# Kernel optimization log

Hardware: AMD Instinct MI355X
Metric: run time of the kernel (lower is better)

## Reference

```python
import jax, jax.numpy as jnp
import numpy as np
import math

B, N, F = 16, 1024, 1024
OUT = 1024

def setup_inputs() -> dict:
    key = jax.random.key(0)
    k1, k2, k3, k4 = jax.random.split(key, 4)
    prott5_emd = jax.random.normal(k1, (B, N, F), dtype=jnp.float32)
    # shared (dense) normalized adjacency, as the original applies one adj to every sample
    adj = jax.random.uniform(k2, (N, N), dtype=jnp.float32)
    adj = adj / jnp.sum(adj, axis=1, keepdims=True)  # row-normalize like a GCN propagation matrix
    h0 = jax.random.normal(k3, (B, N, F), dtype=jnp.float32)
    stdv = 1.0 / math.sqrt(OUT)
    weight = jax.random.uniform(k4, (F, OUT), minval=-stdv, maxval=stdv, dtype=jnp.float32)
    return {"prott5_emd": prott5_emd, "adj": adj, "h0": h0, "weight": weight,
            "lamda": 0.5, "alpha": 0.1, "l": 1}

def reference(prott5_emd, adj, h0, weight, lamda, alpha, l):
    # GraphConvolution (GCNII-style), variant=False, residual=False
    theta = min(1.0, math.log(lamda / l + 1.0))  # static python scalar
    # batched aggregation: adj @ x_i for every sample i  ->  [B, N, F]
    hi = jnp.einsum('nm,bmf->bnf', adj, prott5_emd)
    support = (1.0 - alpha) * hi + alpha * h0          # affine combine with initial features
    out = theta * jnp.einsum('bnf,fo->bno', support, weight) + (1.0 - theta) * support
    return out
```

## Files before the change

### kernel.cpp

```cpp
#include <hip/hip_runtime.h>
#include <hip/hip_bf16.h>

typedef __attribute__((ext_vector_type(8))) short bf16x8;
typedef __attribute__((ext_vector_type(4))) float f32x4;
typedef __attribute__((ext_vector_type(4))) unsigned int u32x4;
typedef __attribute__((ext_vector_type(2))) unsigned int u32x2;

__device__ __forceinline__ float b2f(unsigned short u) {
  unsigned int x = ((unsigned int)u) << 16;
  float f;
  __builtin_memcpy(&f, &x, 4);
  return f;
}
__device__ __forceinline__ unsigned short f2b(float f) {
  __hip_bfloat16 h = __float2bfloat16(f);
  unsigned short u;
  __builtin_memcpy(&u, &h, 2);
  return u;
}

__global__ __launch_bounds__(256) void prep_all(
    const float* __restrict__ X, const float* __restrict__ adj,
    const float* __restrict__ W, unsigned short* __restrict__ XT,
    unsigned short* __restrict__ AJ, unsigned short* __restrict__ WT,
    float theta) {
  const int z = blockIdx.z;
  const int t = threadIdx.x;
  const int r0 = blockIdx.y * 64, c0 = blockIdx.x * 64;

  if (z == 17) {
#pragma unroll
    for (int p = 0; p < 4; ++p) {
      const int id = t + 256 * p;
      const int r = id >> 4, c4 = (id & 15) * 4;
      f32x4 v = *(const f32x4*)(adj + (size_t)(r0 + r) * 1024 + (c0 + c4));
      unsigned short o[4];
#pragma unroll
      for (int j = 0; j < 4; ++j) o[j] = f2b(v[j]);
      u32x2 pk;
      __builtin_memcpy(&pk, o, 8);
      *(u32x2*)(AJ + (size_t)(r0 + r) * 1024 + (c0 + c4)) = pk;
    }
    return;
  }

  if (z == 16) {
    __shared__ float tile[64][65];
#pragma unroll
    for (int p = 0; p < 4; ++p) {
      const int id = t + 256 * p;
      const int r = id >> 4, c4 = (id & 15) * 4;
      f32x4 v = *(const f32x4*)(W + (size_t)(r0 + r) * 1024 + (c0 + c4));
#pragma unroll
      for (int j = 0; j < 4; ++j) tile[r][c4 + j] = v[j];
    }
    __syncthreads();
#pragma unroll
    for (int p = 0; p < 2; ++p) {
      const int id = t + 256 * p;
      const int oc = id >> 3, cr8 = (id & 7) * 8;
      u32x4 v;
      unsigned short* pv = (unsigned short*)&v;
#pragma unroll
      for (int j = 0; j < 8; ++j) {
        const int o = c0 + oc, f = r0 + cr8 + j;
        float val = theta * tile[cr8 + j][oc] + (o == f ? (1.0f - theta) : 0.f);
        pv[j] = f2b(val);
      }
      *(u32x4*)(WT + (size_t)(c0 + oc) * 1024 + (r0 + cr8)) = v;
    }
    return;
  }

  __shared__ unsigned short tile[64][68];
  const float* s = X + (size_t)z * 1024 * 1024;
  unsigned short* d = XT + (size_t)z * 1024 * 1024;
#pragma unroll
  for (int p = 0; p < 4; ++p) {
    const int id = t + 256 * p;
    const int r = id >> 4, c4 = (id & 15) * 4;
    f32x4 v = *(const f32x4*)(s + (size_t)(r0 + r) * 1024 + (c0 + c4));
#pragma unroll
    for (int j = 0; j < 4; ++j) tile[r][c4 + j] = f2b(v[j]);
  }
  __syncthreads();
#pragma unroll
  for (int p = 0; p < 2; ++p) {
    const int id = t + 256 * p;
    const int oc = id >> 3, cr8 = (id & 7) * 8;
    u32x4 v;
    unsigned short* pv = (unsigned short*)&v;
#pragma unroll
    for (int j = 0; j < 8; ++j) pv[j] = tile[cr8 + j][oc];
    *(u32x4*)(d + (size_t)(c0 + oc) * 1024 + (r0 + cr8)) = v;
  }
}

__global__ __launch_bounds__(256, 3) void gemm1(
    const unsigned short* __restrict__ A, const unsigned short* __restrict__ BT,
    const float* __restrict__ E, unsigned short* __restrict__ Cq,
    float c0, float c1) {
  constexpr int NT = 16;
  constexpr size_t NF = 1024ull * 1024ull;
  __shared__ unsigned short Abuf[128 * 64];
  __shared__ unsigned short Bbuf[128 * 64];
  const int bid = blockIdx.x;
  const int nid = (bid & 7) * 128 + (bid >> 3);
  const size_t m0 = (size_t)(nid >> 7) * 128, n0 = (size_t)(nid & 127) * 128;
  const int t = threadIdx.x, lane = t & 63, wv = t >> 6;
  const int wm = (wv >> 1) * 64, wn = (wv & 1) * 64;

  f32x4 acc[4][4];
#pragma unroll
  for (int i = 0; i < 4; ++i)
#pragma unroll
    for (int j = 0; j < 4; ++j) acc[i][j] = (f32x4){0.f, 0.f, 0.f, 0.f};

  for (int tt = 0; tt < NT; ++tt) {
    const int k0 = tt * 64;
#pragma unroll
    for (int l = 0; l < 4; ++l) {
      const int id = l * 256 + t;
      const int rl = id >> 3, c = id & 7;
      const int gc = (c ^ (rl & 7)) << 3;
      const unsigned short* ga = A + (m0 + rl) * 1024 + k0 + gc;
      __builtin_amdgcn_global_load_lds(
          (const __attribute__((address_space(1))) unsigned int*)ga,
          (__attribute__((address_space(3))) unsigned int*)(Abuf + id * 8),
          16, 0, 0);
    }
#pragma unroll
    for (int l = 0; l < 4; ++l) {
      const int id = l * 256 + t;
      const int rl = id >> 3, c = id & 7;
      const int gc = (c ^ (rl & 7)) << 3;
      const unsigned short* gb = BT + (n0 + rl) * 1024 + k0 + gc;
      __builtin_amdgcn_global_load_lds(
          (const __attribute__((address_space(1))) unsigned int*)gb,
          (__attribute__((address_space(3))) unsigned int*)(Bbuf + id * 8),
          16, 0, 0);
    }
    asm volatile("s_waitcnt vmcnt(0)" ::: "memory");
    __builtin_amdgcn_s_barrier();

    bf16x8 breg[4][2];
#pragma unroll
    for (int nj = 0; nj < 4; ++nj)
#pragma unroll
      for (int kk = 0; kk < 2; ++kk) {
        const int row = wn + nj * 16 + (lane & 15);
        const int ch = ((kk * 4 + (lane >> 4)) ^ (row & 7)) << 3;
        breg[nj][kk] = *(const bf16x8*)(Bbuf + row * 64 + ch);
      }
#pragma unroll
    for (int mi = 0; mi < 4; ++mi) {
      bf16x8 ar[2];
#pragma unroll
      for (int kk = 0; kk < 2; ++kk) {
        const int row = wm + mi * 16 + (lane & 15);
        const int ch = ((kk * 4 + (lane >> 4)) ^ (row & 7)) << 3;
        ar[kk] = *(const bf16x8*)(Abuf + row * 64 + ch);
      }
#pragma unroll
      for (int nj = 0; nj < 4; ++nj)
#pragma unroll
        for (int kk = 0; kk < 2; ++kk)
          acc[mi][nj] = __builtin_amdgcn_mfma_f32_16x16x32_bf16(
              ar[kk], breg[nj][kk], acc[mi][nj], 0, 0, 0);
    }
    __builtin_amdgcn_s_barrier();
  }

  const size_t base = (n0 >> 10) * NF + (n0 & 1023) + m0 * 1024;
  float* ldsF = (float*)Abuf;
#pragma unroll
  for (int NH = 0; NH < 2; ++NH) {
    __syncthreads();
    if ((wv & 1) == NH) {
      const int q = lane >> 4;
#pragma unroll
      for (int mi = 0; mi < 4; ++mi)
#pragma unroll
        for (int nj = 0; nj < 4; ++nj)
#pragma unroll
          for (int r = 0; r < 4; ++r) {
            const int row = wm + mi * 16 + q * 4 + r;
            const int col = (nj * 16 + (lane & 15)) ^ (q << 4);
            ldsF[row * 64 + col] = acc[mi][nj][r];
          }
    }
    __syncthreads();
#pragma unroll 4
    for (int it = 0; it < 8; ++it) {
      const int chunk = it * 256 + t;
      const int row = chunk >> 4;
      const int c4 = (chunk & 15) * 4;
      const int sc4 = c4 ^ (((row >> 2) & 3) << 4);
      const f32x4 s = *(const f32x4*)(ldsF + row * 64 + sc4);
      const size_t goff = base + (size_t)row * 1024 + NH * 64 + c4;
      const f32x4 h = *(const f32x4*)(E + goff);
      unsigned short o[4];
#pragma unroll
      for (int j = 0; j < 4; ++j) o[j] = f2b(c0 * s[j] + c1 * h[j]);
      u32x2 pk;
      __builtin_memcpy(&pk, o, 8);
      *(u32x2*)(Cq + goff) = pk;
    }
  }
}

__device__ __forceinline__ void stage_tile16(unsigned short* ldsbase,
                                             const unsigned short* __restrict__ gbase,
                                             size_t rowbase, int half, int k0,
                                             int t, int wv) {
#pragma unroll
  for (int l = 0; l < 2; ++l) {
    const int id = l * 512 + t;
    const int rl = id >> 3, c = id & 7;
    const int gc = (c ^ (rl & 7)) << 3;
    const unsigned short* g = gbase + (rowbase + half * 128 + rl) * 1024 + k0 + gc;
    unsigned short* dst = ldsbase + half * 8192 + (l * 512 + wv * 64) * 8;
    __builtin_amdgcn_global_load_lds(
        (const __attribute__((address_space(1))) unsigned int*)g,
        (__attribute__((address_space(3))) unsigned int*)dst, 16, 0, 0);
  }
}

#define LOAD_A(MH)                                                     \
  {                                                                    \
    const unsigned short* Ard = lds[rd * 2 + 0];                       \
    _Pragma("unroll") for (int mi = 0; mi < 4; ++mi)                   \
        _Pragma("unroll") for (int kk = 0; kk < 2; ++kk) {             \
      const int row = wm + (MH)*64 + mi * 16 + (lane & 15);            \
      const int ch = ((kk * 4 + (lane >> 4)) ^ (row & 7)) << 3;        \
      areg[mi][kk] = *(const bf16x8*)(Ard + row * 64 + ch);            \
    }                                                                  \
  }
#define LOAD_B(NH, BR)                                                 \
  {                                                                    \
    const unsigned short* Brd = lds[rd * 2 + 1];                       \
    _Pragma("unroll") for (int nj = 0; nj < 2; ++nj)                   \
        _Pragma("unroll") for (int kk = 0; kk < 2; ++kk) {             \
      const int row = wn + (NH)*32 + nj * 16 + (lane & 15);            \
      const int ch = ((kk * 4 + (lane >> 4)) ^ (row & 7)) << 3;        \
      BR[nj][kk] = *(const bf16x8*)(Brd + row * 64 + ch);              \
    }                                                                  \
  }
#define MFMA_Q(MH, NH, BR)                                             \
  do {                                                                 \
    __builtin_amdgcn_s_setprio(1);                                     \
    _Pragma("unroll") for (int mi = 0; mi < 4; ++mi)                   \
        _Pragma("unroll") for (int nj = 0; nj < 2; ++nj)               \
            _Pragma("unroll") for (int kk = 0; kk < 2; ++kk)           \
        acc[(MH)*4 + mi][(NH)*2 + nj] =                                \
        __builtin_amdgcn_mfma_f32_16x16x32_bf16(                       \
            areg[mi][kk], BR[nj][kk], acc[(MH)*4 + mi][(NH)*2 + nj],   \
            0, 0, 0);                                                  \
    __builtin_amdgcn_s_setprio(0);                                     \
  } while (0)
#define LGKM0                                          \
  asm volatile("s_waitcnt lgkmcnt(0)" ::: "memory");   \
  __builtin_amdgcn_sched_barrier(0)
#define BAR __builtin_amdgcn_s_barrier()

__global__ __launch_bounds__(512, 2) void gemm2(
    const unsigned short* __restrict__ A, const unsigned short* __restrict__ BT,
    float* __restrict__ Co) {
  constexpr int NT = 16;
  __shared__ unsigned short lds[4][16384];
  const int bid = blockIdx.x;
  const int nid = (bid & 7) * 32 + (bid >> 3);
  const size_t m0 = (size_t)(nid >> 2) * 256, n0 = (size_t)(nid & 3) * 256;
  const int t = threadIdx.x, lane = t & 63, wv = t >> 6;
  const int wm = (wv >> 2) * 128, wn = (wv & 3) * 64;

  f32x4 acc[8][4];
#pragma unroll
  for (int i = 0; i < 8; ++i)
#pragma unroll
    for (int j = 0; j < 4; ++j) acc[i][j] = (f32x4){0.f, 0.f, 0.f, 0.f};
  bf16x8 areg[4][2], b0r[2][2], b1r[2][2];

  stage_tile16(lds[0], A, m0, 0, 0, t, wv);
  stage_tile16(lds[0], A, m0, 1, 0, t, wv);
  stage_tile16(lds[1], BT, n0, 0, 0, t, wv);
  stage_tile16(lds[1], BT, n0, 1, 0, t, wv);
  stage_tile16(lds[3], BT, n0, 0, 64, t, wv);
  stage_tile16(lds[2], A, m0, 0, 64, t, wv);
  asm volatile("s_waitcnt vmcnt(4)" ::: "memory");
  BAR;

  for (int tt = 0; tt < NT; ++tt) {
    const int rd = tt & 1, wr = rd ^ 1;
    LOAD_A(0);
    LOAD_B(0, b0r);
    if (tt + 1 < NT) stage_tile16(lds[wr * 2 + 1], BT, n0, 1, (tt + 1) * 64, t, wv);
    BAR; LGKM0; MFMA_Q(0, 0, b0r); BAR;
    LOAD_B(1, b1r);
    if (tt + 1 < NT) stage_tile16(lds[wr * 2 + 0], A, m0, 1, (tt + 1) * 64, t, wv);
    BAR; LGKM0; MFMA_Q(0, 1, b1r); BAR;
    LOAD_A(1);
    if (tt + 2 < NT) stage_tile16(lds[rd * 2 + 1], BT, n0, 0, (tt + 2) * 64, t, wv);
    BAR; LGKM0; MFMA_Q(1, 1, b1r); BAR;
    if (tt + 2 < NT) stage_tile16(lds[rd * 2 + 0], A, m0, 0, (tt + 2) * 64, t, wv);
    BAR; LGKM0; MFMA_Q(1, 0, b0r);
    asm volatile("s_waitcnt vmcnt(4)" ::: "memory");
    BAR;
  }

  const size_t base = m0 * 1024 + n0;
  float* ldsF = (float*)lds;
#pragma unroll
  for (int MH = 0; MH < 2; ++MH) {
    __syncthreads();
    if ((wv >> 2) == MH) {
      const int q = lane >> 4;
#pragma unroll
      for (int mi = 0; mi < 8; ++mi)
#pragma unroll
        for (int nj = 0; nj < 4; ++nj)
#pragma unroll
          for (int r = 0; r < 4; ++r) {
            const int row = mi * 16 + q * 4 + r;
            const int col = (wn + nj * 16 + (lane & 15)) ^ (q << 4);
            ldsF[row * 256 + col] = acc[mi][nj][r];
          }
    }
    __syncthreads();
#pragma unroll 4
    for (int it = 0; it < 16; ++it) {
      const int chunk = it * 512 + t;
      const int row = chunk >> 6;
      const int c4 = (chunk & 63) * 4;
      const int sc4 = c4 ^ (((row >> 2) & 3) << 4);
      const f32x4 s = *(const f32x4*)(ldsF + row * 256 + sc4);
      *(f32x4*)(Co + base + (size_t)(MH * 128 + row) * 1024 + c4) = s;
    }
  }
}

#undef LOAD_A
#undef LOAD_B
#undef MFMA_Q
#undef LGKM0
#undef BAR

extern "C" void kernel_launch(void* const* d_in, const int* in_sizes, int n_in,
                              void* d_out, int out_size, void* d_ws,
                              size_t ws_size, hipStream_t stream) {
  const float* X = (const float*)d_in[0];
  const float* adj = (const float*)d_in[1];
  const float* h0 = (const float*)d_in[2];
  const float* W = (const float*)d_in[3];
  float* out = (float*)d_out;

  const size_t NF = 1024ull * 1024ull;
  unsigned short* XT = (unsigned short*)d_ws;
  unsigned short* WT = XT + 16 * NF;
  unsigned short* AJ = WT + NF;
  unsigned short* S = AJ + NF;

  const float theta = 0.405465108f;

  prep_all<<<dim3(16, 16, 18), 256, 0, stream>>>(X, adj, W, XT, AJ, WT, theta);

  gemm1<<<dim3(1024), 256, 0, stream>>>(AJ, XT, h0, S, 0.9f, 0.1f);
  gemm2<<<dim3(256), 512, 0, stream>>>(S, WT, out);
}
```

Measured before the change: 119.6 us.

## Enlarge gemm1 tile to 256x128 with 512 threads, write epilogue directly

gemm1 now uses 512-thread blocks covering a 256x128 output tile (8 waves), so each B tile staged in LDS is reused by twice as many rows and half as many blocks are launched. The LDS-staged epilogue that transposed the accumulators for coalesced h0 reads and bf16 stores is replaced by direct per-element reads and writes from the MFMA register layout. Larger tiles cut global traffic for B. The direct epilogue issues scattered 2-byte stores and 4-byte loads, which may coalesce poorly.

New measurement: 113.6 us. -5.0%, faster.

```diff
diff --git a/kernel.cpp b/kernel.cpp
--- a/kernel.cpp
+++ b/kernel.cpp
@@ -96,17 +96,18 @@
   }
 }
 
-__global__ __launch_bounds__(256, 3) void gemm1(
+__global__ __launch_bounds__(512, 4) void gemm1(
     const unsigned short* __restrict__ A, const unsigned short* __restrict__ BT,
     const float* __restrict__ E, unsigned short* __restrict__ Cq,
     float c0, float c1) {
   constexpr int NT = 16;
   constexpr size_t NF = 1024ull * 1024ull;
-  __shared__ unsigned short Abuf[128 * 64];
+  __shared__ unsigned short Abuf[256 * 64];
   __shared__ unsigned short Bbuf[128 * 64];
   const int bid = blockIdx.x;
-  const int nid = (bid & 7) * 128 + (bid >> 3);
-  const size_t m0 = (size_t)(nid >> 7) * 128, n0 = (size_t)(nid & 127) * 128;
+  const int nid = (bid & 7) * 64 + (bid >> 3);
+  const size_t m0 = (size_t)(nid >> 7) * 256;
+  const size_t n0 = (size_t)(nid & 127) * 128;
   const int t = threadIdx.x, lane = t & 63, wv = t >> 6;
   const int wm = (wv >> 1) * 64, wn = (wv & 1) * 64;
 
@@ -118,39 +119,40 @@
 
   for (int tt = 0; tt < NT; ++tt) {
     const int k0 = tt * 64;
+    __syncthreads();
 #pragma unroll
     for (int l = 0; l < 4; ++l) {
-      const int id = l * 256 + t;
+      const int id = l * 512 + t;
       const int rl = id >> 3, c = id & 7;
       const int gc = (c ^ (rl & 7)) << 3;
-      const unsigned short* ga = A + (m0 + rl) * 1024 + k0 + gc;
+      const unsigned short* g = A + (m0 + rl) * 1024 + k0 + gc;
       __builtin_amdgcn_global_load_lds(
-          (const __attribute__((address_space(1))) unsigned int*)ga,
+          (const __attribute__((address_space(1))) unsigned int*)g,
           (__attribute__((address_space(3))) unsigned int*)(Abuf + id * 8),
           16, 0, 0);
     }
 #pragma unroll
-    for (int l = 0; l < 4; ++l) {
-      const int id = l * 256 + t;
+    for (int l = 0; l < 2; ++l) {
+      const int id = l * 512 + t;
       const int rl = id >> 3, c = id & 7;
       const int gc = (c ^ (rl & 7)) << 3;
-      const unsigned short* gb = BT + (n0 + rl) * 1024 + k0 + gc;
+      const unsigned short* g = BT + (n0 + rl) * 1024 + k0 + gc;
       __builtin_amdgcn_global_load_lds(
-          (const __attribute__((address_space(1))) unsigned int*)gb,
+          (const __attribute__((address_space(1))) unsigned int*)g,
           (__attribute__((address_space(3))) unsigned int*)(Bbuf + id * 8),
           16, 0, 0);
     }
     asm volatile("s_waitcnt vmcnt(0)" ::: "memory");
-    __builtin_amdgcn_s_barrier();
-
-    bf16x8 breg[4][2];
+    __syncthreads();
+
+    bf16x8 br[4][2];
 #pragma unroll
     for (int nj = 0; nj < 4; ++nj)
 #pragma unroll
       for (int kk = 0; kk < 2; ++kk) {
         const int row = wn + nj * 16 + (lane & 15);
         const int ch = ((kk * 4 + (lane >> 4)) ^ (row & 7)) << 3;
-        breg[nj][kk] = *(const bf16x8*)(Bbuf + row * 64 + ch);
+        br[nj][kk] = *(const bf16x8*)(Bbuf + row * 64 + ch);
       }
 #pragma unroll
     for (int mi = 0; mi < 4; ++mi) {
@@ -166,45 +168,25 @@
 #pragma unroll
         for (int kk = 0; kk < 2; ++kk)
           acc[mi][nj] = __builtin_amdgcn_mfma_f32_16x16x32_bf16(
-              ar[kk], breg[nj][kk], acc[mi][nj], 0, 0, 0);
-    }
-    __builtin_amdgcn_s_barrier();
+              ar[kk], br[nj][kk], acc[mi][nj], 0, 0, 0);
+    }
   }
 
   const size_t base = (n0 >> 10) * NF + (n0 & 1023) + m0 * 1024;
-  float* ldsF = (float*)Abuf;
-#pragma unroll
-  for (int NH = 0; NH < 2; ++NH) {
-    __syncthreads();
-    if ((wv & 1) == NH) {
-      const int q = lane >> 4;
-#pragma unroll
-      for (int mi = 0; mi < 4; ++mi)
-#pragma unroll
-        for (int nj = 0; nj < 4; ++nj)
-#pragma unroll
-          for (int r = 0; r < 4; ++r) {
-            const int row = wm + mi * 16 + q * 4 + r;
-            const int col = (nj * 16 + (lane & 15)) ^ (q << 4);
-            ldsF[row * 64 + col] = acc[mi][nj][r];
-          }
-    }
-    __syncthreads();
-#pragma unroll 4
-    for (int it = 0; it < 8; ++it) {
-      const int chunk = it * 256 + t;
-      const int row = chunk >> 4;
-      const int c4 = (chunk & 15) * 4;
-      const int sc4 = c4 ^ (((row >> 2) & 3) << 4);
-      const f32x4 s = *(const f32x4*)(ldsF + row * 64 + sc4);
-      const size_t goff = base + (size_t)row * 1024 + NH * 64 + c4;
-      const f32x4 h = *(const f32x4*)(E + goff);
-      unsigned short o[4];
-#pragma unroll
-      for (int j = 0; j < 4; ++j) o[j] = f2b(c0 * s[j] + c1 * h[j]);
-      u32x2 pk;
-      __builtin_memcpy(&pk, o, 8);
-      *(u32x2*)(Cq + goff) = pk;
+  const float* Eb = E + base;
+  unsigned short* Cb = Cq + base;
+#pragma unroll
+  for (int mi = 0; mi < 4; ++mi) {
+#pragma unroll
+    for (int r = 0; r < 4; ++r) {
+      const int lrow = wm + mi * 16 + (lane >> 4) * 4 + r;
+#pragma unroll
+      for (int nj = 0; nj < 4; ++nj) {
+        const int lcol = wn + nj * 16 + (lane & 15);
+        const float v =
+            c0 * acc[mi][nj][r] + c1 * Eb[(size_t)lrow * 1024 + lcol];
+        Cb[(size_t)lrow * 1024 + lcol] = f2b(v);
+      }
     }
   }
 }
@@ -364,6 +346,6 @@
 
   prep_all<<<dim3(16, 16, 18), 256, 0, stream>>>(X, adj, W, XT, AJ, WT, theta);
 
-  gemm1<<<dim3(1024), 256, 0, stream>>>(AJ, XT, h0, S, 0.9f, 0.1f);
+  gemm1<<<dim3(512), 512, 0, stream>>>(AJ, XT, h0, S, 0.9f, 0.1f);
   gemm2<<<dim3(256), 512, 0, stream>>>(S, WT, out);
 }
```
